# Kernel optimization log

Measured on AMD Instinct MI355X. Metric: run time of the kernel, lower is better.

Reference implementation:

```python
import jax, jax.numpy as jnp
import numpy as np

T, B, IN, H, L = 512, 64, 1024, 1024, 2


def setup_inputs() -> dict:
    key = jax.random.key(0)
    ks = jax.random.split(key, 7)
    s = 1.0 / np.sqrt(H)
    return {
        "x": jax.random.normal(ks[0], (T, B, IN), jnp.float32),
        "h0": jax.random.normal(ks[1], (L, B, H), jnp.float32) * 0.1,
        "c0": jax.random.normal(ks[2], (L, B, H), jnp.float32) * 0.1,
        "W0": jax.random.uniform(ks[3], (4 * H, IN + H), jnp.float32, -s, s),
        "b0": jax.random.uniform(ks[4], (4 * H,), jnp.float32, -s, s),
        "W1": jax.random.uniform(ks[5], (4 * H, H + H), jnp.float32, -s, s),
        "b1": jax.random.uniform(ks[6], (4 * H,), jnp.float32, -s, s),
    }


def _cell(xin, h, c, W, b):
    # xin: [B, D], h/c: [B, H], W: [4H, D+H], b: [4H]
    xh = jnp.concatenate([xin, h], axis=1)
    gates = xh @ W.T + b
    i, f, g, o = jnp.split(gates, 4, axis=1)  # ingate, forgetgate, cellgate, outgate
    i = jax.nn.sigmoid(i)
    f = jax.nn.sigmoid(f)
    g = jnp.tanh(g)
    o = jax.nn.sigmoid(o)
    cy = i * g + f * c
    hy = o * jnp.tanh(cy)
    return hy, cy


def reference(x, h0, c0, W0, b0, W1, b1):
    Ws = [(W0, b0), (W1, b1)]

    def step(carry, xt):
        h, c = carry  # each [L, B, H]
        xin = xt
        hs, cs = [], []
        for k in range(L):
            W, b = Ws[k]
            hy, cy = _cell(xin, h[k], c[k], W, b)
            hs.append(hy)
            cs.append(cy)
            xin = hy
        return (jnp.stack(hs), jnp.stack(cs)), xin  # xin is last-layer h

    (h, c), hlast = jax.lax.scan(step, (h0, c0), x)
    return hlast, h, c
```

## Files before the change

### kernel.cpp

```cpp
#include <hip/hip_runtime.h>
#include <hip/hip_bf16.h>
#include <stdint.h>

#define TT 512
#define BB 64
#define HH 1024
#define BH 65536
#define KD 2048

typedef __attribute__((ext_vector_type(8))) short short8;
typedef __attribute__((ext_vector_type(4))) float f32x4;

__device__ __forceinline__ unsigned short f2bf(float f) {
  union { float f; unsigned int u; } v; v.f = f;
  unsigned int r = v.u + 0x7fffu + ((v.u >> 16) & 1u);
  return (unsigned short)(r >> 16);
}
__device__ __forceinline__ float fsig(float x)  { return 1.0f / (1.0f + __expf(-x)); }
__device__ __forceinline__ float ftanhf(float x){ return 1.0f - 2.0f / (__expf(2.0f * x) + 1.0f); }

__global__ void cvt_x_kernel(const float* __restrict__ x, unsigned short* __restrict__ xbf) {
  const int n4 = (TT * BB * 1024) / 4;
  int stride = gridDim.x * blockDim.x;
  for (int i = blockIdx.x * blockDim.x + threadIdx.x; i < n4; i += stride) {
    float4 v = ((const float4*)x)[i];
    unsigned long long p = (unsigned long long)f2bf(v.x)
        | ((unsigned long long)f2bf(v.y) << 16)
        | ((unsigned long long)f2bf(v.z) << 32)
        | ((unsigned long long)f2bf(v.w) << 48);
    ((unsigned long long*)xbf)[i] = p;
  }
}

__global__ void cvt_w_kernel(const float* __restrict__ W, unsigned short* __restrict__ Ws) {
  int idx = blockIdx.x * blockDim.x + threadIdx.x;
  int hi = idx & 3;
  int nr = (idx >> 2) & 31;
  int kk = (idx >> 7) & 63;
  int g  = idx >> 13;
  int q  = nr & 3;
  int jl = (nr >> 2) & 3;
  int nt = nr >> 4;
  int grow = (q << 10) + (g << 3) + (nt << 2) + jl;
  int k = ((kk < 32) ? (kk << 5) : (1024 + ((kk - 32) << 5))) + (hi << 3);
  const float* src = W + (size_t)grow * KD + k;
  float4 v0 = ((const float4*)src)[0];
  float4 v1 = ((const float4*)src)[1];
  unsigned long long p0 = (unsigned long long)f2bf(v0.x)
      | ((unsigned long long)f2bf(v0.y) << 16)
      | ((unsigned long long)f2bf(v0.z) << 32)
      | ((unsigned long long)f2bf(v0.w) << 48);
  unsigned long long p1 = (unsigned long long)f2bf(v1.x)
      | ((unsigned long long)f2bf(v1.y) << 16)
      | ((unsigned long long)f2bf(v1.z) << 32)
      | ((unsigned long long)f2bf(v1.w) << 48);
  unsigned long long* dst = (unsigned long long*)(Ws + ((size_t)g << 16) + (kk << 10) + (nr << 5) + (hi << 3));
  dst[0] = p0;
  dst[1] = p1;
}

__global__ void init_state_kernel(const float* __restrict__ h0in,
                                  unsigned short* h0s0, unsigned short* h1s0) {
  int i = blockIdx.x * blockDim.x + threadIdx.x;
  h0s0[i] = f2bf(h0in[i]);
  h1s0[i] = f2bf(h0in[BH + i]);
}

#define GLD(p)    __hip_atomic_load((p),  __ATOMIC_RELAXED, __HIP_MEMORY_SCOPE_AGENT)
#define GST(p, v) __hip_atomic_store((p), (v), __ATOMIC_RELAXED, __HIP_MEMORY_SCOPE_AGENT)

__device__ __forceinline__ void poll128(int* base) {
  for (;;) {
    int s = 0;
#pragma unroll
    for (int j = 0; j < 8; j++)
      s += GLD(base + (j << 6));
    if (s >= 128) return;
    __builtin_amdgcn_s_sleep(1);
  }
}

__global__ __launch_bounds__(512, 2) void lstm_persist(
    const unsigned short* __restrict__ W0s, const unsigned short* __restrict__ W1s,
    const float* __restrict__ b0, const float* __restrict__ b1,
    const unsigned short* __restrict__ xbf,
    unsigned short* h0hist, unsigned short* h1hist,
    const float* __restrict__ c0in, float* out, int* cnt)
{
  __shared__ short8 wlds[8192];
  __shared__ f32x4 pbuf[2][4][2][64];
  const int tid = threadIdx.x;
  const int bid = blockIdx.x;
  const int layer = bid >> 7;
  const int g = bid & 127;

  const unsigned short* Ws = layer ? W1s : W0s;
  const float* bias = layer ? b1 : b0;
  int* const cnt0 = cnt;
  int* const cnt1 = cnt + (TT << 9);

  {
    const short8* wsrc = (const short8*)(Ws + ((size_t)g << 16));
#pragma unroll
    for (int it = 0; it < 16; it++)
      wlds[tid + (it << 9)] = wsrc[tid + (it << 9)];
  }

  const int lane = tid & 63;
  const int w  = tid >> 6;
  const bool isA = (w < 4);
  const int mt = w & 3;
  const int m0 = mt << 4;
  const int n  = lane & 15;
  const int hi = lane >> 4;
  const short8* bbase0 = wlds + ((n << 2) + hi);
  const short8* bbase1 = wlds + (((16 + n) << 2) + hi);
  const int rowoff = ((m0 + n) << 10) + (hi << 3);
  const int m = m0 + n;
  const int col0 = (g << 3) + hi;
  const int col1 = col0 + 4;

  unsigned short* const myhist = (layer == 0) ? h0hist : h1hist;
  int* const mycnt = (layer == 0) ? cnt0 : cnt1;

  float bq[2][4];
  float creg[2];
  if (!isA) {
#pragma unroll
    for (int nt2 = 0; nt2 < 2; nt2++) {
      int col = nt2 ? col1 : col0;
#pragma unroll
      for (int qg = 0; qg < 4; qg++)
        bq[nt2][qg] = bias[(qg << 10) + col];
      creg[nt2] = c0in[(size_t)layer * BH + (m << 10) + col];
    }
  }
  __syncthreads();

  if (isA) {
    if (layer == 1) {
      if (lane == 0) poll128(cnt0);
      asm volatile("" ::: "memory");
    }
    const unsigned short* asrc = ((layer == 0) ? xbf : h0hist + (size_t)BH) + rowoff;
    short8 ha[8];
#pragma unroll
    for (int j = 0; j < 8; j++) ha[j] = *(const short8*)(asrc + (j << 5));
    f32x4 a0 = {0.f, 0.f, 0.f, 0.f}, a1 = {0.f, 0.f, 0.f, 0.f};
#pragma unroll
    for (int blk = 0; blk < 4; blk++) {
#pragma unroll
      for (int j = 0; j < 8; j++) {
        int kk = (blk << 3) + j;
        a0 = __builtin_amdgcn_mfma_f32_16x16x32_bf16(bbase0[kk << 7], ha[j], a0, 0, 0, 0);
        a1 = __builtin_amdgcn_mfma_f32_16x16x32_bf16(bbase1[kk << 7], ha[j], a1, 0, 0, 0);
        if (blk < 3) ha[j] = *(const short8*)(asrc + ((kk + 8) << 5));
      }
    }
    pbuf[0][mt][0][lane] = a0;
    pbuf[0][mt][1][lane] = a1;
  }
  __syncthreads();

  for (int s = 0; s < TT; s++) {
    float hsv[2];

    if (isA) {
      if (s + 1 < TT) {
        if (layer == 1) {
          if (lane == 0) poll128(cnt0 + ((s + 1) << 9));
          asm volatile("" ::: "memory");
        }
        const unsigned short* asrc = ((layer == 0) ? xbf + (size_t)(s + 1) * BH
                                                   : h0hist + (size_t)(s + 2) * BH) + rowoff;
        short8 ha[8];
#pragma unroll
        for (int j = 0; j < 8; j++) ha[j] = *(const short8*)(asrc + (j << 5));
        f32x4 a0 = {0.f, 0.f, 0.f, 0.f}, a1 = {0.f, 0.f, 0.f, 0.f};
#pragma unroll
        for (int blk = 0; blk < 4; blk++) {
#pragma unroll
          for (int j = 0; j < 8; j++) {
            int kk = (blk << 3) + j;
            a0 = __builtin_amdgcn_mfma_f32_16x16x32_bf16(bbase0[kk << 7], ha[j], a0, 0, 0, 0);
            a1 = __builtin_amdgcn_mfma_f32_16x16x32_bf16(bbase1[kk << 7], ha[j], a1, 0, 0, 0);
            if (blk < 3) ha[j] = *(const short8*)(asrc + ((kk + 8) << 5));
          }
        }
        int buf = (s + 1) & 1;
        pbuf[buf][mt][0][lane] = a0;
        pbuf[buf][mt][1][lane] = a1;
      }
    } else {
      if (s >= 1) {
        if (lane == 0) poll128(mycnt + ((s - 1) << 9));
        asm volatile("" ::: "memory");
      }
      f32x4 acc0 = pbuf[s & 1][mt][0][lane];
      f32x4 acc1 = pbuf[s & 1][mt][1][lane];
      const unsigned short* inB = myhist + (size_t)s * BH + rowoff;
      short8 ha[8];
#pragma unroll
      for (int j = 0; j < 8; j++) ha[j] = *(const short8*)(inB + (j << 5));
#pragma unroll
      for (int blk = 0; blk < 4; blk++) {
#pragma unroll
        for (int j = 0; j < 8; j++) {
          int kk = (blk << 3) + j;
          acc0 = __builtin_amdgcn_mfma_f32_16x16x32_bf16(bbase0[(32 + kk) << 7], ha[j], acc0, 0, 0, 0);
          acc1 = __builtin_amdgcn_mfma_f32_16x16x32_bf16(bbase1[(32 + kk) << 7], ha[j], acc1, 0, 0, 0);
          if (blk < 3) ha[j] = *(const short8*)(inB + ((kk + 8) << 5));
        }
      }

      unsigned short* hb = myhist + (size_t)(s + 1) * BH;
#pragma unroll
      for (int nt2 = 0; nt2 < 2; nt2++) {
        f32x4 acc = nt2 ? acc1 : acc0;
        const int col = nt2 ? col1 : col0;
        float ig = fsig(acc[0] + bq[nt2][0]);
        float fg = fsig(acc[1] + bq[nt2][1]);
        float gg = ftanhf(acc[2] + bq[nt2][2]);
        float og = fsig(acc[3] + bq[nt2][3]);
        float cn = ig * gg + fg * creg[nt2];
        float hn = og * ftanhf(cn);
        creg[nt2] = cn;
        hsv[nt2] = hn;
        GST(hb + (m << 10) + col, f2bf(hn));
      }
    }

    __syncthreads();
    if (tid == 0) atomicAdd(mycnt + (s << 9) + ((g & 7) << 6), 1);

    if (!isA) {
#pragma unroll
      for (int nt2 = 0; nt2 < 2; nt2++) {
        const int col = nt2 ? col1 : col0;
        const int idx = (m << 10) + col;
        float hn = hsv[nt2];
        if (layer == 1) {
          out[(size_t)s * BH + idx] = hn;
          if (s == TT - 1) {
            out[(size_t)TT * BH + BH + idx] = hn;
            out[(size_t)TT * BH + 3 * BH + idx] = creg[nt2];
          }
        } else if (s == TT - 1) {
          out[(size_t)TT * BH + idx] = hn;
          out[(size_t)TT * BH + 2 * BH + idx] = creg[nt2];
        }
      }
    }
  }
}

extern "C" void kernel_launch(void* const* d_in, const int* in_sizes, int n_in,
                              void* d_out, int out_size, void* d_ws, size_t ws_size,
                              hipStream_t stream) {
  (void)in_sizes; (void)n_in; (void)out_size; (void)ws_size;
  const float* x    = (const float*)d_in[0];
  const float* h0in = (const float*)d_in[1];
  const float* c0in = (const float*)d_in[2];
  const float* W0   = (const float*)d_in[3];
  const float* b0   = (const float*)d_in[4];
  const float* W1   = (const float*)d_in[5];
  const float* b1   = (const float*)d_in[6];
  float* out = (float*)d_out;

  char* ws = (char*)d_ws;
  const size_t HIST = (size_t)(TT + 1) * BH * sizeof(unsigned short);
  unsigned short* Xbf    = (unsigned short*)(ws);
  unsigned short* W0s    = (unsigned short*)(ws + 67108864);
  unsigned short* W1s    = (unsigned short*)(ws + 83886080);
  unsigned short* h0hist = (unsigned short*)(ws + 100663296);
  unsigned short* h1hist = (unsigned short*)(ws + 100663296 + HIST);
  int* cnt               = (int*)(ws + 100663296 + 2 * HIST);

  const size_t CNT_BYTES = (size_t)2 * TT * 512 * sizeof(int);
  hipMemsetAsync(cnt, 0, CNT_BYTES, stream);
  cvt_x_kernel<<<2048, 256, 0, stream>>>(x, Xbf);
  cvt_w_kernel<<<4096, 256, 0, stream>>>(W0, W0s);
  cvt_w_kernel<<<4096, 256, 0, stream>>>(W1, W1s);
  init_state_kernel<<<256, 256, 0, stream>>>(h0in, h0hist, h1hist);

  lstm_persist<<<256, 512, 0, stream>>>(W0s, W1s, b0, b1, Xbf,
                                        h0hist, h1hist, c0in, out, cnt);
}
```

Before: 4.699 ms.

## Replace per-step block barrier with LDS flag handshakes between producer and consumer waves

Removes the __syncthreads at the end of each timestep. The A-waves (input projection) and B-waves (recurrent part plus activations) now coordinate through workgroup-scope LDS counters: seal flags mark a filled pbuf half, consume counters allow that half to be reused, and a drain counter lets one wave publish the global step counter once all B-waves' stores have completed. The aim is to let A-waves run ahead and overlap with B-waves instead of lockstepping. It also loads all 32 A-operand fragments up front instead of the rolling 8-register prefetch. This raises register pressure and relies on hand-written spin waits and s_waitcnt ordering for correctness.

```diff
diff --git a/kernel.cpp b/kernel.cpp
--- a/kernel.cpp
+++ b/kernel.cpp
@@ -68,6 +68,8 @@
 
 #define GLD(p)    __hip_atomic_load((p),  __ATOMIC_RELAXED, __HIP_MEMORY_SCOPE_AGENT)
 #define GST(p, v) __hip_atomic_store((p), (v), __ATOMIC_RELAXED, __HIP_MEMORY_SCOPE_AGENT)
+#define LLD(p)    __hip_atomic_load((p),  __ATOMIC_RELAXED, __HIP_MEMORY_SCOPE_WORKGROUP)
+#define LADD(p)   __hip_atomic_fetch_add((p), 1, __ATOMIC_RELAXED, __HIP_MEMORY_SCOPE_WORKGROUP)
 
 __device__ __forceinline__ void poll128(int* base) {
   for (;;) {
@@ -89,6 +91,9 @@
 {
   __shared__ short8 wlds[8192];
   __shared__ f32x4 pbuf[2][4][2][64];
+  __shared__ int sealA[2];
+  __shared__ int consB[2];
+  __shared__ int bdrain;
   const int tid = threadIdx.x;
   const int bid = blockIdx.x;
   const int layer = bid >> 7;
@@ -98,6 +103,8 @@
   const float* bias = layer ? b1 : b0;
   int* const cnt0 = cnt;
   int* const cnt1 = cnt + (TT << 9);
+
+  if (tid == 0) { sealA[0] = 4; sealA[1] = 0; consB[0] = 0; consB[1] = 0; bdrain = 0; }
 
   {
     const short8* wsrc = (const short8*)(Ws + ((size_t)g << 16));
@@ -143,19 +150,14 @@
       asm volatile("" ::: "memory");
     }
     const unsigned short* asrc = ((layer == 0) ? xbf : h0hist + (size_t)BH) + rowoff;
-    short8 ha[8];
-#pragma unroll
-    for (int j = 0; j < 8; j++) ha[j] = *(const short8*)(asrc + (j << 5));
+    short8 xa[32];
+#pragma unroll
+    for (int j = 0; j < 32; j++) xa[j] = *(const short8*)(asrc + (j << 5));
     f32x4 a0 = {0.f, 0.f, 0.f, 0.f}, a1 = {0.f, 0.f, 0.f, 0.f};
 #pragma unroll
-    for (int blk = 0; blk < 4; blk++) {
-#pragma unroll
-      for (int j = 0; j < 8; j++) {
-        int kk = (blk << 3) + j;
-        a0 = __builtin_amdgcn_mfma_f32_16x16x32_bf16(bbase0[kk << 7], ha[j], a0, 0, 0, 0);
-        a1 = __builtin_amdgcn_mfma_f32_16x16x32_bf16(bbase1[kk << 7], ha[j], a1, 0, 0, 0);
-        if (blk < 3) ha[j] = *(const short8*)(asrc + ((kk + 8) << 5));
-      }
+    for (int kk = 0; kk < 32; kk++) {
+      a0 = __builtin_amdgcn_mfma_f32_16x16x32_bf16(bbase0[kk << 7], xa[kk], a0, 0, 0, 0);
+      a1 = __builtin_amdgcn_mfma_f32_16x16x32_bf16(bbase1[kk << 7], xa[kk], a1, 0, 0, 0);
     }
     pbuf[0][mt][0][lane] = a0;
     pbuf[0][mt][1][lane] = a1;
@@ -163,56 +165,55 @@
   __syncthreads();
 
   for (int s = 0; s < TT; s++) {
-    float hsv[2];
-
     if (isA) {
       if (s + 1 < TT) {
+        const int buf = (s + 1) & 1;
         if (layer == 1) {
           if (lane == 0) poll128(cnt0 + ((s + 1) << 9));
           asm volatile("" ::: "memory");
         }
+        const int needC = 4 * ((s + 1) >> 1);
+        if (lane == 0 && needC) { while (LLD(&consB[buf]) < needC) {} }
+        asm volatile("" ::: "memory");
         const unsigned short* asrc = ((layer == 0) ? xbf + (size_t)(s + 1) * BH
                                                    : h0hist + (size_t)(s + 2) * BH) + rowoff;
-        short8 ha[8];
-#pragma unroll
-        for (int j = 0; j < 8; j++) ha[j] = *(const short8*)(asrc + (j << 5));
+        short8 xa[32];
+#pragma unroll
+        for (int j = 0; j < 32; j++) xa[j] = *(const short8*)(asrc + (j << 5));
         f32x4 a0 = {0.f, 0.f, 0.f, 0.f}, a1 = {0.f, 0.f, 0.f, 0.f};
 #pragma unroll
-        for (int blk = 0; blk < 4; blk++) {
-#pragma unroll
-          for (int j = 0; j < 8; j++) {
-            int kk = (blk << 3) + j;
-            a0 = __builtin_amdgcn_mfma_f32_16x16x32_bf16(bbase0[kk << 7], ha[j], a0, 0, 0, 0);
-            a1 = __builtin_amdgcn_mfma_f32_16x16x32_bf16(bbase1[kk << 7], ha[j], a1, 0, 0, 0);
-            if (blk < 3) ha[j] = *(const short8*)(asrc + ((kk + 8) << 5));
-          }
+        for (int kk = 0; kk < 32; kk++) {
+          a0 = __builtin_amdgcn_mfma_f32_16x16x32_bf16(bbase0[kk << 7], xa[kk], a0, 0, 0, 0);
+          a1 = __builtin_amdgcn_mfma_f32_16x16x32_bf16(bbase1[kk << 7], xa[kk], a1, 0, 0, 0);
         }
-        int buf = (s + 1) & 1;
         pbuf[buf][mt][0][lane] = a0;
         pbuf[buf][mt][1][lane] = a1;
+        asm volatile("s_waitcnt lgkmcnt(0)" ::: "memory");
+        if (lane == 0) LADD(&sealA[buf]);
       }
     } else {
+      const int needS = 4 * ((s + 2) >> 1);
+      if (lane == 0) { while (LLD(&sealA[s & 1]) < needS) {} }
+      asm volatile("" ::: "memory");
+      f32x4 acc0 = pbuf[s & 1][mt][0][lane];
+      f32x4 acc1 = pbuf[s & 1][mt][1][lane];
+      asm volatile("s_waitcnt lgkmcnt(0)" ::: "memory");
+      if (lane == 0) LADD(&consB[s & 1]);
       if (s >= 1) {
         if (lane == 0) poll128(mycnt + ((s - 1) << 9));
         asm volatile("" ::: "memory");
       }
-      f32x4 acc0 = pbuf[s & 1][mt][0][lane];
-      f32x4 acc1 = pbuf[s & 1][mt][1][lane];
       const unsigned short* inB = myhist + (size_t)s * BH + rowoff;
-      short8 ha[8];
-#pragma unroll
-      for (int j = 0; j < 8; j++) ha[j] = *(const short8*)(inB + (j << 5));
-#pragma unroll
-      for (int blk = 0; blk < 4; blk++) {
-#pragma unroll
-        for (int j = 0; j < 8; j++) {
-          int kk = (blk << 3) + j;
-          acc0 = __builtin_amdgcn_mfma_f32_16x16x32_bf16(bbase0[(32 + kk) << 7], ha[j], acc0, 0, 0, 0);
-          acc1 = __builtin_amdgcn_mfma_f32_16x16x32_bf16(bbase1[(32 + kk) << 7], ha[j], acc1, 0, 0, 0);
-          if (blk < 3) ha[j] = *(const short8*)(inB + ((kk + 8) << 5));
-        }
-      }
-
+      short8 ha[32];
+#pragma unroll
+      for (int j = 0; j < 32; j++) ha[j] = *(const short8*)(inB + (j << 5));
+#pragma unroll
+      for (int kk = 0; kk < 32; kk++) {
+        acc0 = __builtin_amdgcn_mfma_f32_16x16x32_bf16(bbase0[(32 + kk) << 7], ha[kk], acc0, 0, 0, 0);
+        acc1 = __builtin_amdgcn_mfma_f32_16x16x32_bf16(bbase1[(32 + kk) << 7], ha[kk], acc1, 0, 0, 0);
+      }
+
+      float hsv[2];
       unsigned short* hb = myhist + (size_t)(s + 1) * BH;
 #pragma unroll
       for (int nt2 = 0; nt2 < 2; nt2++) {
@@ -228,12 +229,14 @@
         hsv[nt2] = hn;
         GST(hb + (m << 10) + col, f2bf(hn));
       }
-    }
-
-    __syncthreads();
-    if (tid == 0) atomicAdd(mycnt + (s << 9) + ((g & 7) << 6), 1);
-
-    if (!isA) {
+
+      asm volatile("s_waitcnt vmcnt(0)" ::: "memory");
+      if (lane == 0) LADD(&bdrain);
+      if (w == 4 && lane == 0) {
+        while (LLD(&bdrain) < 4 * (s + 1)) {}
+        atomicAdd(mycnt + (s << 9) + ((g & 7) << 6), 1);
+      }
+
 #pragma unroll
       for (int nt2 = 0; nt2 < 2; nt2++) {
         const int col = nt2 ? col1 : col0;
```

New measurement: 6.689 ms. 42.3% more time.

## Block the h-history layout and move fp32 output writes to a finalize kernel

Applied to the files above, without the earlier changes.

Stores the bf16 hidden-state history in a blocked layout, so each workgroup's per-step h writes land in one contiguous segment and the MFMA operand loads read 8-column chunks at a stride. The per-step fp32 writes of the last-layer h to the output are removed from the persistent recurrent loop. A separate finalize kernel now expands the bf16 history to fp32 for the sequence output and the final h states. This takes scattered global stores off the latency-critical step loop, at the cost of an extra pass over the history. The returned h values also become bf16-rounded instead of exact fp32.

```diff
diff --git a/kernel.cpp b/kernel.cpp
--- a/kernel.cpp
+++ b/kernel.cpp
@@ -15,6 +15,9 @@
   union { float f; unsigned int u; } v; v.f = f;
   unsigned int r = v.u + 0x7fffu + ((v.u >> 16) & 1u);
   return (unsigned short)(r >> 16);
+}
+__device__ __forceinline__ float bf2f(unsigned short u) {
+  union { unsigned int u; float f; } v; v.u = ((unsigned int)u) << 16; return v.f;
 }
 __device__ __forceinline__ float fsig(float x)  { return 1.0f / (1.0f + __expf(-x)); }
 __device__ __forceinline__ float ftanhf(float x){ return 1.0f - 2.0f / (__expf(2.0f * x) + 1.0f); }
@@ -62,8 +65,33 @@
 __global__ void init_state_kernel(const float* __restrict__ h0in,
                                   unsigned short* h0s0, unsigned short* h1s0) {
   int i = blockIdx.x * blockDim.x + threadIdx.x;
-  h0s0[i] = f2bf(h0in[i]);
-  h1s0[i] = f2bf(h0in[BH + i]);
+  int m = i >> 10, c = i & 1023;
+  int dst = ((c >> 3) << 9) + (m << 3) + (c & 7);
+  h0s0[dst] = f2bf(h0in[i]);
+  h1s0[dst] = f2bf(h0in[BH + i]);
+}
+
+__global__ void finalize_kernel(const unsigned short* __restrict__ h0hist,
+                                const unsigned short* __restrict__ h1hist,
+                                float* __restrict__ out) {
+  const size_t NCH = (size_t)(TT + 2) * (BH / 8);
+  size_t stride = (size_t)gridDim.x * blockDim.x;
+  for (size_t i = (size_t)blockIdx.x * blockDim.x + threadIdx.x; i < NCH; i += stride) {
+    int p  = (int)(i >> 13);
+    int ci = (int)(i & 8191);
+    int cb = ci >> 6, m = ci & 63;
+    const unsigned short* src;
+    size_t dbase;
+    if (p < TT)       { src = h1hist + (size_t)(p + 1) * BH; dbase = (size_t)p * BH; }
+    else if (p == TT) { src = h0hist + (size_t)TT * BH;      dbase = (size_t)TT * BH; }
+    else              { src = h1hist + (size_t)TT * BH;      dbase = (size_t)TT * BH + BH; }
+    const unsigned short* sp = src + ((size_t)ci << 3);
+    ushort4 v0 = ((const ushort4*)sp)[0];
+    ushort4 v1 = ((const ushort4*)sp)[1];
+    float* dp = out + dbase + (m << 10) + (cb << 3);
+    *(float4*)(dp)     = make_float4(bf2f(v0.x), bf2f(v0.y), bf2f(v0.z), bf2f(v0.w));
+    *(float4*)(dp + 4) = make_float4(bf2f(v1.x), bf2f(v1.y), bf2f(v1.z), bf2f(v1.w));
+  }
 }
 
 #define GLD(p)    __hip_atomic_load((p),  __ATOMIC_RELAXED, __HIP_MEMORY_SCOPE_AGENT)
@@ -115,8 +143,9 @@
   const int hi = lane >> 4;
   const short8* bbase0 = wlds + ((n << 2) + hi);
   const short8* bbase1 = wlds + (((16 + n) << 2) + hi);
-  const int rowoff = ((m0 + n) << 10) + (hi << 3);
   const int m = m0 + n;
+  const int rowoff = (m << 10) + (hi << 3);
+  const int bro = ((hi << 6) + m) << 3;
   const int col0 = (g << 3) + hi;
   const int col1 = col0 + 4;
 
@@ -142,20 +171,35 @@
       if (lane == 0) poll128(cnt0);
       asm volatile("" ::: "memory");
     }
-    const unsigned short* asrc = ((layer == 0) ? xbf : h0hist + (size_t)BH) + rowoff;
-    short8 ha[8];
-#pragma unroll
-    for (int j = 0; j < 8; j++) ha[j] = *(const short8*)(asrc + (j << 5));
     f32x4 a0 = {0.f, 0.f, 0.f, 0.f}, a1 = {0.f, 0.f, 0.f, 0.f};
-#pragma unroll
-    for (int blk = 0; blk < 4; blk++) {
-#pragma unroll
-      for (int j = 0; j < 8; j++) {
-        int kk = (blk << 3) + j;
-        a0 = __builtin_amdgcn_mfma_f32_16x16x32_bf16(bbase0[kk << 7], ha[j], a0, 0, 0, 0);
-        a1 = __builtin_amdgcn_mfma_f32_16x16x32_bf16(bbase1[kk << 7], ha[j], a1, 0, 0, 0);
-        if (blk < 3) ha[j] = *(const short8*)(asrc + ((kk + 8) << 5));
-      }
+    if (layer == 0) {
+      const unsigned short* asrc = xbf + rowoff;
+      short8 ha[8];
+#pragma unroll
+      for (int j = 0; j < 8; j++) ha[j] = *(const short8*)(asrc + (j << 5));
+#pragma unroll
+      for (int blk = 0; blk < 4; blk++)
+#pragma unroll
+        for (int j = 0; j < 8; j++) {
+          int kk = (blk << 3) + j;
+          a0 = __builtin_amdgcn_mfma_f32_16x16x32_bf16(bbase0[kk << 7], ha[j], a0, 0, 0, 0);
+          a1 = __builtin_amdgcn_mfma_f32_16x16x32_bf16(bbase1[kk << 7], ha[j], a1, 0, 0, 0);
+          if (blk < 3) ha[j] = *(const short8*)(asrc + ((kk + 8) << 5));
+        }
+    } else {
+      const unsigned short* asrc = h0hist + (size_t)BH + bro;
+      short8 ha[8];
+#pragma unroll
+      for (int j = 0; j < 8; j++) ha[j] = *(const short8*)(asrc + (j << 11));
+#pragma unroll
+      for (int blk = 0; blk < 4; blk++)
+#pragma unroll
+        for (int j = 0; j < 8; j++) {
+          int kk = (blk << 3) + j;
+          a0 = __builtin_amdgcn_mfma_f32_16x16x32_bf16(bbase0[kk << 7], ha[j], a0, 0, 0, 0);
+          a1 = __builtin_amdgcn_mfma_f32_16x16x32_bf16(bbase1[kk << 7], ha[j], a1, 0, 0, 0);
+          if (blk < 3) ha[j] = *(const short8*)(asrc + ((kk + 8) << 11));
+        }
     }
     pbuf[0][mt][0][lane] = a0;
     pbuf[0][mt][1][lane] = a1;
@@ -163,29 +207,39 @@
   __syncthreads();
 
   for (int s = 0; s < TT; s++) {
-    float hsv[2];
-
     if (isA) {
       if (s + 1 < TT) {
-        if (layer == 1) {
+        f32x4 a0 = {0.f, 0.f, 0.f, 0.f}, a1 = {0.f, 0.f, 0.f, 0.f};
+        if (layer == 0) {
+          const unsigned short* asrc = xbf + (size_t)(s + 1) * BH + rowoff;
+          short8 ha[8];
+#pragma unroll
+          for (int j = 0; j < 8; j++) ha[j] = *(const short8*)(asrc + (j << 5));
+#pragma unroll
+          for (int blk = 0; blk < 4; blk++)
+#pragma unroll
+            for (int j = 0; j < 8; j++) {
+              int kk = (blk << 3) + j;
+              a0 = __builtin_amdgcn_mfma_f32_16x16x32_bf16(bbase0[kk << 7], ha[j], a0, 0, 0, 0);
+              a1 = __builtin_amdgcn_mfma_f32_16x16x32_bf16(bbase1[kk << 7], ha[j], a1, 0, 0, 0);
+              if (blk < 3) ha[j] = *(const short8*)(asrc + ((kk + 8) << 5));
+            }
+        } else {
           if (lane == 0) poll128(cnt0 + ((s + 1) << 9));
           asm volatile("" ::: "memory");
-        }
-        const unsigned short* asrc = ((layer == 0) ? xbf + (size_t)(s + 1) * BH
-                                                   : h0hist + (size_t)(s + 2) * BH) + rowoff;
-        short8 ha[8];
-#pragma unroll
-        for (int j = 0; j < 8; j++) ha[j] = *(const short8*)(asrc + (j << 5));
-        f32x4 a0 = {0.f, 0.f, 0.f, 0.f}, a1 = {0.f, 0.f, 0.f, 0.f};
-#pragma unroll
-        for (int blk = 0; blk < 4; blk++) {
-#pragma unroll
-          for (int j = 0; j < 8; j++) {
-            int kk = (blk << 3) + j;
-            a0 = __builtin_amdgcn_mfma_f32_16x16x32_bf16(bbase0[kk << 7], ha[j], a0, 0, 0, 0);
-            a1 = __builtin_amdgcn_mfma_f32_16x16x32_bf16(bbase1[kk << 7], ha[j], a1, 0, 0, 0);
-            if (blk < 3) ha[j] = *(const short8*)(asrc + ((kk + 8) << 5));
-          }
+          const unsigned short* asrc = h0hist + (size_t)(s + 2) * BH + bro;
+          short8 ha[8];
+#pragma unroll
+          for (int j = 0; j < 8; j++) ha[j] = *(const short8*)(asrc + (j << 11));
+#pragma unroll
+          for (int blk = 0; blk < 4; blk++)
+#pragma unroll
+            for (int j = 0; j < 8; j++) {
+              int kk = (blk << 3) + j;
+              a0 = __builtin_amdgcn_mfma_f32_16x16x32_bf16(bbase0[kk << 7], ha[j], a0, 0, 0, 0);
+              a1 = __builtin_amdgcn_mfma_f32_16x16x32_bf16(bbase1[kk << 7], ha[j], a1, 0, 0, 0);
+              if (blk < 3) ha[j] = *(const short8*)(asrc + ((kk + 8) << 11));
+            }
         }
         int buf = (s + 1) & 1;
         pbuf[buf][mt][0][lane] = a0;
@@ -198,26 +252,24 @@
       }
       f32x4 acc0 = pbuf[s & 1][mt][0][lane];
       f32x4 acc1 = pbuf[s & 1][mt][1][lane];
-      const unsigned short* inB = myhist + (size_t)s * BH + rowoff;
+      const unsigned short* inB = myhist + (size_t)s * BH + bro;
       short8 ha[8];
 #pragma unroll
-      for (int j = 0; j < 8; j++) ha[j] = *(const short8*)(inB + (j << 5));
-#pragma unroll
-      for (int blk = 0; blk < 4; blk++) {
+      for (int j = 0; j < 8; j++) ha[j] = *(const short8*)(inB + (j << 11));
+#pragma unroll
+      for (int blk = 0; blk < 4; blk++)
 #pragma unroll
         for (int j = 0; j < 8; j++) {
           int kk = (blk << 3) + j;
           acc0 = __builtin_amdgcn_mfma_f32_16x16x32_bf16(bbase0[(32 + kk) << 7], ha[j], acc0, 0, 0, 0);
           acc1 = __builtin_amdgcn_mfma_f32_16x16x32_bf16(bbase1[(32 + kk) << 7], ha[j], acc1, 0, 0, 0);
-          if (blk < 3) ha[j] = *(const short8*)(inB + ((kk + 8) << 5));
+          if (blk < 3) ha[j] = *(const short8*)(inB + ((kk + 8) << 11));
         }
-      }
-
-      unsigned short* hb = myhist + (size_t)(s + 1) * BH;
+
+      unsigned short* hbb = myhist + (size_t)(s + 1) * BH + (((g << 6) + m) << 3);
 #pragma unroll
       for (int nt2 = 0; nt2 < 2; nt2++) {
         f32x4 acc = nt2 ? acc1 : acc0;
-        const int col = nt2 ? col1 : col0;
         float ig = fsig(acc[0] + bq[nt2][0]);
         float fg = fsig(acc[1] + bq[nt2][1]);
         float gg = ftanhf(acc[2] + bq[nt2][2]);
@@ -225,30 +277,18 @@
         float cn = ig * gg + fg * creg[nt2];
         float hn = og * ftanhf(cn);
         creg[nt2] = cn;
-        hsv[nt2] = hn;
-        GST(hb + (m << 10) + col, f2bf(hn));
+        GST(hbb + (nt2 << 2) + hi, f2bf(hn));
       }
     }
 
     __syncthreads();
     if (tid == 0) atomicAdd(mycnt + (s << 9) + ((g & 7) << 6), 1);
 
-    if (!isA) {
+    if (!isA && s == TT - 1) {
 #pragma unroll
       for (int nt2 = 0; nt2 < 2; nt2++) {
         const int col = nt2 ? col1 : col0;
-        const int idx = (m << 10) + col;
-        float hn = hsv[nt2];
-        if (layer == 1) {
-          out[(size_t)s * BH + idx] = hn;
-          if (s == TT - 1) {
-            out[(size_t)TT * BH + BH + idx] = hn;
-            out[(size_t)TT * BH + 3 * BH + idx] = creg[nt2];
-          }
-        } else if (s == TT - 1) {
-          out[(size_t)TT * BH + idx] = hn;
-          out[(size_t)TT * BH + 2 * BH + idx] = creg[nt2];
-        }
+        out[(size_t)TT * BH + (size_t)(2 + layer) * BH + (m << 10) + col] = creg[nt2];
       }
     }
   }
@@ -285,4 +325,6 @@
 
   lstm_persist<<<256, 512, 0, stream>>>(W0s, W1s, b0, b1, Xbf,
                                         h0hist, h1hist, c0in, out, cnt);
-}
+
+  finalize_kernel<<<2048, 256, 0, stream>>>(h0hist, h1hist, out);
+}
```

New measurement: 4.203 ms. -10.5%, faster.
